# Optimization experiments

Hardware: AMD Instinct MI355X
Metric: run time of the kernel (lower is better)

Reference implementation:

```python
import jax, jax.numpy as jnp
import numpy as np


def _forward(x, conv_w, conv_b, lin_w, lin_b, W_in, conv1d_w, conv1d_b, W_x, W_dt, b_dt, A_log, Dp, W_out, We, be, Wa, ba, Wq, bq):
    B, _, H, Wd = x.shape
    E = conv_w.shape[0]
    # conv stem: Conv2d(k=3, pad=1) -> flatten(2) -> Linear(H*W -> img_size)
    z = jax.lax.conv_general_dilated(x, conv_w, (1, 1), [(1, 1), (1, 1)],
                                     dimension_numbers=('NCHW', 'OIHW', 'NCHW'))
    z = z + conv_b[None, :, None, None]
    z = z.reshape(B, E, H * Wd)                              # [B,E,HW]
    z = jnp.einsum('ben,mn->bem', z, lin_w) + lin_b          # [B,E,L]
    u = z.transpose(2, 0, 1)                                 # [L,B,E]: Mamba sees batch=L, seq=B
    # ---- Mamba block (mamba_ssm reference math) ----
    di = W_in.shape[0] // 2
    xz = u @ W_in.T                                          # [L,seq,2*di]
    xm, zg = xz[..., :di], xz[..., di:]
    K = conv1d_w.shape[-1]
    xc = jax.lax.conv_general_dilated(xm.transpose(0, 2, 1), conv1d_w, (1,), [(K - 1, 0)],
                                      dimension_numbers=('NCH', 'OIH', 'NCH'),
                                      feature_group_count=di)  # causal depthwise conv
    xs = jax.nn.silu((xc + conv1d_b[None, :, None]).transpose(0, 2, 1))  # [L,seq,di]
    dbl = xs @ W_x.T                                         # [L,seq,dt_rank+2S]
    dt_rank = W_dt.shape[1]
    S = A_log.shape[1]
    delta = jax.nn.softplus(dbl[..., :dt_rank] @ W_dt.T + b_dt)          # [L,seq,di]
    Bm = dbl[..., dt_rank:dt_rank + S]                       # [L,seq,S]
    Cm = dbl[..., dt_rank + S:]                              # [L,seq,S]
    A = -jnp.exp(A_log)                                      # [di,S]

    def step(h, t):
        d_t, b_t, c_t, x_t = t                               # [L,di],[L,S],[L,S],[L,di]
        h = jnp.exp(d_t[:, :, None] * A) * h + (d_t * x_t)[:, :, None] * b_t[:, None, :]
        return h, jnp.einsum('lds,ls->ld', h, c_t)

    h0 = jnp.zeros((u.shape[0], di, S), xs.dtype)
    _, ys = jax.lax.scan(step, h0, (delta.transpose(1, 0, 2), Bm.transpose(1, 0, 2),
                                    Cm.transpose(1, 0, 2), xs.transpose(1, 0, 2)))
    y = (ys.transpose(1, 0, 2) + xs * Dp) * jax.nn.silu(zg)  # [L,seq,di]
    out = y @ W_out.T                                        # [L,seq,E]
    feat = out[-1]                                           # [B,E] (last 'mamba batch' row)
    return feat @ We.T + be, feat @ Wa.T + ba, feat @ Wq.T + bq


def setup_inputs() -> dict:
    key = jax.random.key(0)
    ks = jax.random.split(key, 16)
    B, C, IMG, E, S, K = 512, 1, 32, 128, 256, 4
    di, dt_rank = 2 * E, 8
    sc = 0.02
    return {
        'x': jax.random.normal(ks[0], (B, C, IMG, IMG), jnp.float32),
        'conv_w': sc * jax.random.normal(ks[1], (E, C, 3, 3), jnp.float32),
        'conv_b': jnp.zeros((E,), jnp.float32),
        'lin_w': sc * jax.random.normal(ks[2], (IMG, IMG * IMG), jnp.float32),
        'lin_b': jnp.zeros((IMG,), jnp.float32),
        'W_in': sc * jax.random.normal(ks[3], (2 * di, E), jnp.float32),
        'conv1d_w': sc * jax.random.normal(ks[4], (di, 1, K), jnp.float32),
        'conv1d_b': jnp.zeros((di,), jnp.float32),
        'W_x': sc * jax.random.normal(ks[5], (dt_rank + 2 * S, di), jnp.float32),
        'W_dt': sc * jax.random.normal(ks[6], (di, dt_rank), jnp.float32),
        'b_dt': 0.1 * jax.random.normal(ks[7], (di,), jnp.float32),
        'A_log': jnp.log(jnp.broadcast_to(jnp.arange(1, S + 1, dtype=jnp.float32), (di, S))),
        'Dp': jnp.ones((di,), jnp.float32),
        'W_out': sc * jax.random.normal(ks[8], (E, di), jnp.float32),
        'We': sc * jax.random.normal(ks[9], (1, E), jnp.float32),
        'be': jnp.zeros((1,), jnp.float32),
        'Wa': sc * jax.random.normal(ks[10], (3, E), jnp.float32),
        'ba': jnp.zeros((3,), jnp.float32),
        'Wq': sc * jax.random.normal(ks[11], (4, E), jnp.float32),
        'bq': jnp.zeros((4,), jnp.float32),
    }


def reference(x, conv_w, conv_b, lin_w, lin_b, W_in, conv1d_w, conv1d_b, W_x, W_dt, b_dt, A_log, Dp, W_out, We, be, Wa, ba, Wq, bq):
    return _forward(x, conv_w, conv_b, lin_w, lin_b, W_in, conv1d_w, conv1d_b, W_x,
                    W_dt, b_dt, A_log, Dp, W_out, We, be, Wa, ba, Wq, bq)
```

## Files before the change

kernel.cpp:

```cpp
#include <hip/hip_runtime.h>
#include <math.h>

#define BATCH 512
#define E     128
#define DI    256
#define S     256
#define DTR   8
#define KCONV 4

__device__ __forceinline__ float silu_f(float v) {
    return v / (1.0f + __expf(-v));
}

__global__ __launch_bounds__(256) void k1_conv_lin(
    const float* __restrict__ x, const float* __restrict__ conv_w,
    const float* __restrict__ conv_b, const float* __restrict__ lin_w,
    const float* __restrict__ lin_b, float* __restrict__ u31)
{
    const int b = blockIdx.x;
    const int tid = threadIdx.x;
    __shared__ float lw[1024];
    __shared__ float red[10][4];
    __shared__ float Tsh[10];

    for (int i = tid; i < 1024; i += 256) lw[i] = lin_w[31 * 1024 + i];
    __syncthreads();

    float acc[10];
#pragma unroll
    for (int k = 0; k < 10; k++) acc[k] = 0.0f;

    const float* xb = x + (size_t)b * 1024;
    for (int p = tid; p < 1024; p += 256) {
        const float xv = xb[p];
        const int h = p >> 5, w = p & 31;
#pragma unroll
        for (int i = 0; i < 3; i++) {
            const int hh = h - (i - 1);
            if (hh < 0 || hh > 31) continue;
#pragma unroll
            for (int j = 0; j < 3; j++) {
                const int ww = w - (j - 1);
                if (ww < 0 || ww > 31) continue;
                acc[i * 3 + j] += xv * lw[hh * 32 + ww];
            }
        }
        acc[9] += lw[p];
    }

    const int wv = tid >> 6, ln = tid & 63;
#pragma unroll
    for (int k = 0; k < 10; k++) {
#pragma unroll
        for (int m = 1; m < 64; m <<= 1) acc[k] += __shfl_xor(acc[k], m, 64);
    }
    if (ln == 0) {
#pragma unroll
        for (int k = 0; k < 10; k++) red[k][wv] = acc[k];
    }
    __syncthreads();
    if (tid < 10) Tsh[tid] = red[tid][0] + red[tid][1] + red[tid][2] + red[tid][3];
    __syncthreads();

    if (tid < E) {
        const int e = tid;
        float v = lin_b[31] + conv_b[e] * Tsh[9];
#pragma unroll
        for (int k = 0; k < 9; k++) v += conv_w[e * 9 + k] * Tsh[k];
        u31[b * E + e] = v;
    }
}

__global__ __launch_bounds__(256) void k2a_win(
    const float* __restrict__ u31, const float* __restrict__ W_in,
    float* __restrict__ xm, float* __restrict__ zg)
{
    const int bb = blockIdx.x * 4;
    const int tid = threadIdx.x;
    __shared__ float u[4][E];
    for (int i = tid; i < 4 * E; i += 256) u[i >> 7][i & 127] = u31[bb * E + i];
    __syncthreads();

    const int jj = blockIdx.y * 256 + tid;
    float acc[4];
#pragma unroll
    for (int r = 0; r < 4; r++) acc[r] = 0.0f;
    const float* wrow = W_in + jj * E;
#pragma unroll 4
    for (int e = 0; e < E; e++) {
        const float w = wrow[e];
#pragma unroll
        for (int r = 0; r < 4; r++) acc[r] += w * u[r][e];
    }
    if (jj < 256) {
#pragma unroll
        for (int r = 0; r < 4; r++) xm[(bb + r) * DI + jj] = acc[r];
    } else {
#pragma unroll
        for (int r = 0; r < 4; r++) zg[(bb + r) * DI + (jj - 256)] = acc[r];
    }
}

__global__ __launch_bounds__(256) void k2b_conv_wx(
    const float* __restrict__ xm, const float* __restrict__ conv1d_w,
    const float* __restrict__ conv1d_b, const float* __restrict__ W_x,
    const float* __restrict__ W_dt, const float* __restrict__ b_dt,
    float* __restrict__ xs_g, float* __restrict__ delta_g,
    float* __restrict__ Bm, float* __restrict__ Cm)
{
    const int bb = blockIdx.x * 8;
    const int by = blockIdx.y;
    const int tid = threadIdx.x;
    __shared__ float xs[8][DI];
    __shared__ float dtin[8][8];

    for (int idx = tid; idx < 8 * DI; idx += 256) {
        const int r = idx >> 8, c = idx & 255;
        const int b = bb + r;
        float a = 0.0f;
#pragma unroll
        for (int k = 0; k < KCONV; k++) {
            const int src = b - 3 + k;
            if (src >= 0) a += xm[src * DI + c] * conv1d_w[c * KCONV + k];
        }
        a += conv1d_b[c];
        const float s = silu_f(a);
        xs[r][c] = s;
        if (by == 0) xs_g[b * DI + c] = s;
    }
    __syncthreads();

    for (int jj = by * 260 + tid; jj < (by + 1) * 260; jj += 256) {
        float acc[8];
#pragma unroll
        for (int r = 0; r < 8; r++) acc[r] = 0.0f;
        const float* wrow = W_x + jj * DI;
#pragma unroll 4
        for (int c = 0; c < DI; c++) {
            const float w = wrow[c];
#pragma unroll
            for (int r = 0; r < 8; r++) acc[r] += w * xs[r][c];
        }
#pragma unroll
        for (int r = 0; r < 8; r++) {
            const int b = bb + r;
            if (jj < DTR)          dtin[r][jj] = acc[r];
            else if (jj < DTR + S) Bm[b * S + (jj - DTR)] = acc[r];
            else                   Cm[b * S + (jj - DTR - S)] = acc[r];
        }
    }
    __syncthreads();

    if (by == 0) {
        const int d = tid;
        const float bd = b_dt[d];
#pragma unroll
        for (int r = 0; r < 8; r++) {
            float a = bd;
#pragma unroll
            for (int q = 0; q < DTR; q++) a += dtin[r][q] * W_dt[d * DTR + q];
            const float sp = (a > 20.0f) ? a : log1pf(__expf(a));
            delta_g[(bb + r) * DI + d] = sp;
        }
    }
}

template <int NCv>
__global__ __launch_bounds__(256) void k3a_local(
    const float* __restrict__ A_log, const float* __restrict__ delta,
    const float* __restrict__ xs, const float* __restrict__ Bm,
    const float* __restrict__ Cm, float* __restrict__ y,
    float* __restrict__ hloc, float* __restrict__ Dchunk)
{
    constexpr int TCv = BATCH / NCv;
    const int tid = threadIdx.x;
    const int wv = tid >> 6, ln = tid & 63;
    const int d = blockIdx.x * 4 + wv;
    const int c = blockIdx.y;
    const int s0 = ln * 4;
    const int t0 = c * TCv;

    const float4 al = *(const float4*)(A_log + d * S + s0);
    float4 A;
    A.x = -__expf(al.x); A.y = -__expf(al.y);
    A.z = -__expf(al.z); A.w = -__expf(al.w);

    float4 h = make_float4(0.f, 0.f, 0.f, 0.f);
    float cd = 0.0f;
    float pr[8];

    for (int tb = 0; tb < TCv; tb += 8) {
#pragma unroll
        for (int i = 0; i < 8; i++) {
            const int tt = t0 + tb + i;
            const float dd = delta[tt * DI + d];
            cd += dd;
            const float u = dd * xs[tt * DI + d];
            const float4 B = *(const float4*)(Bm + tt * S + s0);
            const float4 C = *(const float4*)(Cm + tt * S + s0);
            h.x = __expf(dd * A.x) * h.x + u * B.x;
            h.y = __expf(dd * A.y) * h.y + u * B.y;
            h.z = __expf(dd * A.z) * h.z + u * B.z;
            h.w = __expf(dd * A.w) * h.w + u * B.w;
            pr[i] = h.x * C.x + h.y * C.y + h.z * C.z + h.w * C.w;
        }
#pragma unroll
        for (int i = 0; i < 8; i++) {
#pragma unroll
            for (int m = 1; m < 64; m <<= 1) pr[i] += __shfl_xor(pr[i], m, 64);
        }
        if (ln == 0) {
#pragma unroll
            for (int i = 0; i < 8; i++) y[(t0 + tb + i) * DI + d] = pr[i];
        }
    }

    *(float4*)(hloc + ((size_t)(c * DI + d)) * S + s0) = h;
    if (ln == 0) Dchunk[c * DI + d] = cd;
}

template <int NCv>
__global__ __launch_bounds__(256) void k3b_carry(
    const float* __restrict__ A_log, const float* __restrict__ hloc,
    const float* __restrict__ Dchunk, float* __restrict__ hin)
{
    const int d = blockIdx.x;
    const int s = threadIdx.x;
    const float A = -__expf(A_log[d * S + s]);

    float h = 0.0f;
    float hf = hloc[((size_t)(0 * DI + d)) * S + s];
    float Dc = Dchunk[0 * DI + d];
    for (int c = 1; c < NCv; c++) {
        float hf_n = 0.0f, Dc_n = 0.0f;
        if (c < NCv - 1) {
            hf_n = hloc[((size_t)(c * DI + d)) * S + s];
            Dc_n = Dchunk[c * DI + d];
        }
        h = hf + __expf(A * Dc) * h;
        hin[((size_t)(c * DI + d)) * S + s] = h;
        hf = hf_n; Dc = Dc_n;
    }
}

template <int NCv>
__global__ __launch_bounds__(256) void k3c_fix(
    const float* __restrict__ A_log, const float* __restrict__ delta,
    const float* __restrict__ Cm, const float* __restrict__ hin,
    float* __restrict__ y)
{
    constexpr int TCv = BATCH / NCv;
    const int tid = threadIdx.x;
    const int wv = tid >> 6, ln = tid & 63;
    const int d = blockIdx.x * 4 + wv;
    const int c = blockIdx.y + 1;
    const int s0 = ln * 4;
    const int t0 = c * TCv;

    const float4 al = *(const float4*)(A_log + d * S + s0);
    float4 A;
    A.x = -__expf(al.x); A.y = -__expf(al.y);
    A.z = -__expf(al.z); A.w = -__expf(al.w);

    const float4 hi = *(const float4*)(hin + ((size_t)(c * DI + d)) * S + s0);

    float cd = 0.0f;
    float pr[8];

    for (int tb = 0; tb < TCv; tb += 8) {
#pragma unroll
        for (int i = 0; i < 8; i++) {
            const int tt = t0 + tb + i;
            const float dd = delta[tt * DI + d];
            cd += dd;
            const float4 C = *(const float4*)(Cm + tt * S + s0);
            const float fx = hi.x * __expf(cd * A.x);
            const float fy = hi.y * __expf(cd * A.y);
            const float fz = hi.z * __expf(cd * A.z);
            const float fw = hi.w * __expf(cd * A.w);
            pr[i] = fx * C.x + fy * C.y + fz * C.z + fw * C.w;
        }
#pragma unroll
        for (int i = 0; i < 8; i++) {
#pragma unroll
            for (int m = 1; m < 64; m <<= 1) pr[i] += __shfl_xor(pr[i], m, 64);
        }
        if (ln == 0) {
#pragma unroll
            for (int i = 0; i < 8; i++) {
                const int tt = t0 + tb + i;
                y[tt * DI + d] += pr[i];
            }
        }
    }
}

__global__ __launch_bounds__(256) void k4_heads(
    const float* __restrict__ y, const float* __restrict__ xs,
    const float* __restrict__ Dp, const float* __restrict__ zg,
    const float* __restrict__ W_out,
    const float* __restrict__ We, const float* __restrict__ be,
    const float* __restrict__ Wa, const float* __restrict__ ba,
    const float* __restrict__ Wq, const float* __restrict__ bq,
    float* __restrict__ out)
{
    const int b = blockIdx.x;
    const int tid = threadIdx.x;
    __shared__ float yf[DI];
    __shared__ float feat[E];

    const float z = zg[b * DI + tid];
    yf[tid] = (y[b * DI + tid] + xs[b * DI + tid] * Dp[tid]) * silu_f(z);
    __syncthreads();

    if (tid < E) {
        float a = 0.0f;
#pragma unroll 4
        for (int dd = 0; dd < DI; dd++) a += yf[dd] * W_out[tid * DI + dd];
        feat[tid] = a;
    }
    __syncthreads();

    if (tid < 8) {
        const float* wrow;
        float bias;
        int dst;
        if (tid == 0)      { wrow = We;                  bias = be[0];       dst = b; }
        else if (tid < 4)  { wrow = Wa + (tid - 1) * E;  bias = ba[tid - 1]; dst = 512 + b * 3 + (tid - 1); }
        else               { wrow = Wq + (tid - 4) * E;  bias = bq[tid - 4]; dst = 2048 + b * 4 + (tid - 4); }
        float a = bias;
#pragma unroll 4
        for (int e = 0; e < E; e++) a += feat[e] * wrow[e];
        out[dst] = a;
    }
}

template <int NCv>
static void launch_scan(const float* A_log, const float* delta, const float* xs,
                        const float* Bm, const float* Cm, float* y,
                        float* hloc, float* hin, float* Dchunk, hipStream_t stream)
{
    k3a_local<NCv><<<dim3(64, NCv), 256, 0, stream>>>(A_log, delta, xs, Bm, Cm, y, hloc, Dchunk);
    k3b_carry<NCv><<<256, 256, 0, stream>>>(A_log, hloc, Dchunk, hin);
    k3c_fix<NCv><<<dim3(64, NCv - 1), 256, 0, stream>>>(A_log, delta, Cm, hin, y);
}

extern "C" void kernel_launch(void* const* d_in, const int* in_sizes, int n_in,
                              void* d_out, int out_size, void* d_ws, size_t ws_size,
                              hipStream_t stream)
{
    const float* x        = (const float*)d_in[0];
    const float* conv_w   = (const float*)d_in[1];
    const float* conv_b   = (const float*)d_in[2];
    const float* lin_w    = (const float*)d_in[3];
    const float* lin_b    = (const float*)d_in[4];
    const float* W_in     = (const float*)d_in[5];
    const float* conv1d_w = (const float*)d_in[6];
    const float* conv1d_b = (const float*)d_in[7];
    const float* W_x      = (const float*)d_in[8];
    const float* W_dt     = (const float*)d_in[9];
    const float* b_dt     = (const float*)d_in[10];
    const float* A_log    = (const float*)d_in[11];
    const float* Dp       = (const float*)d_in[12];
    const float* W_out    = (const float*)d_in[13];
    const float* We       = (const float*)d_in[14];
    const float* be       = (const float*)d_in[15];
    const float* Wa       = (const float*)d_in[16];
    const float* ba       = (const float*)d_in[17];
    const float* Wq       = (const float*)d_in[18];
    const float* bq       = (const float*)d_in[19];
    float* out = (float*)d_out;

    float* ws = (float*)d_ws;
    float* u31   = ws;
    float* xm    = u31 + 512 * 128;
    float* zg    = xm  + 512 * 256;
    float* xs    = zg  + 512 * 256;
    float* delta = xs  + 512 * 256;
    float* Bm    = delta + 512 * 256;
    float* Cm    = Bm  + 512 * 256;
    float* y     = Cm  + 512 * 256;
    float* tail  = y   + 512 * 256;

    const size_t base_floats = (size_t)(tail - ws);

    k1_conv_lin<<<512, 256, 0, stream>>>(x, conv_w, conv_b, lin_w, lin_b, u31);
    k2a_win<<<dim3(128, 2), 256, 0, stream>>>(u31, W_in, xm, zg);
    k2b_conv_wx<<<dim3(64, 2), 256, 0, stream>>>(xm, conv1d_w, conv1d_b, W_x, W_dt, b_dt,
                                                 xs, delta, Bm, Cm);

    const size_t avail = ws_size / 4 - base_floats;
    if (avail >= (size_t)2 * 32 * DI * S + 32 * DI) {
        float* hloc = tail;
        float* hin  = hloc + (size_t)32 * DI * S;
        float* Dch  = hin  + (size_t)32 * DI * S;
        launch_scan<32>(A_log, delta, xs, Bm, Cm, y, hloc, hin, Dch, stream);
    } else if (avail >= (size_t)2 * 16 * DI * S + 16 * DI) {
        float* hloc = tail;
        float* hin  = hloc + (size_t)16 * DI * S;
        float* Dch  = hin  + (size_t)16 * DI * S;
        launch_scan<16>(A_log, delta, xs, Bm, Cm, y, hloc, hin, Dch, stream);
    } else {
        float* hloc = tail;
        float* hin  = hloc + (size_t)8 * DI * S;
        float* Dch  = hin  + (size_t)8 * DI * S;
        launch_scan<8>(A_log, delta, xs, Bm, Cm, y, hloc, hin, Dch, stream);
    }

    k4_heads<<<512, 256, 0, stream>>>(y, xs, Dp, zg, W_out, We, be, Wa, ba, Wq, bq, out);
}
```

Baseline: 200.3 us.

## Transpose weights on device for coalesced GEMV reads and re-grid projection kernels

Adds a per-call kernel that transposes W_in, W_x, W_dt, W_out and the conv1d weights into workspace, so the matvec loops read weight rows coalesced across threads instead of strided per-thread rows. It also re-grids k2a and k2b (more blocks, one output per thread with a row index per wave), processes two batch rows per block in the heads kernel, and vectorizes the conv stem loads with float4. The aim is better memory coalescing and occupancy in the small projection kernels. The cost is an extra launch plus transpose traffic on every call, and the reduced per-thread reuse of the shared-memory rows.

```diff
diff --git a/kernel.cpp b/kernel.cpp
--- a/kernel.cpp
+++ b/kernel.cpp
@@ -7,9 +7,31 @@
 #define S     256
 #define DTR   8
 #define KCONV 4
+#define JWX   520
 
 __device__ __forceinline__ float silu_f(float v) {
     return v / (1.0f + __expf(-v));
+}
+
+__global__ __launch_bounds__(256) void kT_transpose(
+    const float* __restrict__ W_in, const float* __restrict__ W_x,
+    const float* __restrict__ W_dt, const float* __restrict__ W_out,
+    const float* __restrict__ c1w,
+    float* __restrict__ W_inT, float* __restrict__ W_xT,
+    float* __restrict__ W_dtT, float* __restrict__ W_outT,
+    float* __restrict__ c1wT)
+{
+    const int bid = blockIdx.x;
+    const float* src; float* dst; int J, K, j0;
+    if (bid < 9)       { src = W_x;   dst = W_xT;   J = JWX; K = DI;  j0 = bid * 64; }
+    else if (bid < 17) { src = W_in;  dst = W_inT;  J = 512; K = E;   j0 = (bid - 9) * 64; }
+    else if (bid < 19) { src = W_out; dst = W_outT; J = E;   K = DI;  j0 = (bid - 17) * 64; }
+    else if (bid < 23) { src = W_dt;  dst = W_dtT;  J = DI;  K = DTR; j0 = (bid - 19) * 64; }
+    else               { src = c1w;   dst = c1wT;   J = DI;  K = KCONV; j0 = (bid - 23) * 64; }
+    const int j = j0 + (threadIdx.x & 63);
+    if (j >= J) return;
+    for (int c = threadIdx.x >> 6; c < K; c += 4)
+        dst[c * J + j] = src[j * K + c];
 }
 
 __global__ __launch_bounds__(256) void k1_conv_lin(
@@ -23,17 +45,22 @@
     __shared__ float red[10][4];
     __shared__ float Tsh[10];
 
-    for (int i = tid; i < 1024; i += 256) lw[i] = lin_w[31 * 1024 + i];
+    const float4 lv = ((const float4*)(lin_w + 31 * 1024))[tid];
+    ((float4*)lw)[tid] = lv;
     __syncthreads();
 
     float acc[10];
 #pragma unroll
     for (int k = 0; k < 10; k++) acc[k] = 0.0f;
 
-    const float* xb = x + (size_t)b * 1024;
-    for (int p = tid; p < 1024; p += 256) {
-        const float xv = xb[p];
-        const int h = p >> 5, w = p & 31;
+    const float4 xv = ((const float4*)(x + (size_t)b * 1024))[tid];
+    const int p0 = tid * 4;
+    const int h = p0 >> 5, w0 = p0 & 31;
+    const float xa[4] = {xv.x, xv.y, xv.z, xv.w};
+#pragma unroll
+    for (int k = 0; k < 4; k++) {
+        const float xval = xa[k];
+        const int w = w0 + k;
 #pragma unroll
         for (int i = 0; i < 3; i++) {
             const int hh = h - (i - 1);
@@ -42,11 +69,11 @@
             for (int j = 0; j < 3; j++) {
                 const int ww = w - (j - 1);
                 if (ww < 0 || ww > 31) continue;
-                acc[i * 3 + j] += xv * lw[hh * 32 + ww];
+                acc[i * 3 + j] += xval * lw[hh * 32 + ww];
             }
         }
-        acc[9] += lw[p];
-    }
+    }
+    acc[9] = lv.x + lv.y + lv.z + lv.w;
 
     const int wv = tid >> 6, ln = tid & 63;
 #pragma unroll
@@ -72,7 +99,7 @@
 }
 
 __global__ __launch_bounds__(256) void k2a_win(
-    const float* __restrict__ u31, const float* __restrict__ W_in,
+    const float* __restrict__ u31, const float* __restrict__ W_inT,
     float* __restrict__ xm, float* __restrict__ zg)
 {
     const int bb = blockIdx.x * 4;
@@ -81,86 +108,67 @@
     for (int i = tid; i < 4 * E; i += 256) u[i >> 7][i & 127] = u31[bb * E + i];
     __syncthreads();
 
-    const int jj = blockIdx.y * 256 + tid;
-    float acc[4];
-#pragma unroll
-    for (int r = 0; r < 4; r++) acc[r] = 0.0f;
-    const float* wrow = W_in + jj * E;
-#pragma unroll 4
-    for (int e = 0; e < E; e++) {
-        const float w = wrow[e];
-#pragma unroll
-        for (int r = 0; r < 4; r++) acc[r] += w * u[r][e];
-    }
-    if (jj < 256) {
-#pragma unroll
-        for (int r = 0; r < 4; r++) xm[(bb + r) * DI + jj] = acc[r];
-    } else {
-#pragma unroll
-        for (int r = 0; r < 4; r++) zg[(bb + r) * DI + (jj - 256)] = acc[r];
-    }
+    const int r = tid >> 6;
+    const int j = blockIdx.y * 64 + (tid & 63);
+    float a = 0.0f;
+#pragma unroll 8
+    for (int e = 0; e < E; e++) a += u[r][e] * W_inT[e * 512 + j];
+    if (j < 256) xm[(bb + r) * DI + j] = a;
+    else         zg[(bb + r) * DI + (j - 256)] = a;
 }
 
 __global__ __launch_bounds__(256) void k2b_conv_wx(
-    const float* __restrict__ xm, const float* __restrict__ conv1d_w,
-    const float* __restrict__ conv1d_b, const float* __restrict__ W_x,
-    const float* __restrict__ W_dt, const float* __restrict__ b_dt,
+    const float* __restrict__ xm, const float* __restrict__ c1wT,
+    const float* __restrict__ conv1d_b, const float* __restrict__ W_xT,
+    const float* __restrict__ W_dtT, const float* __restrict__ b_dt,
     float* __restrict__ xs_g, float* __restrict__ delta_g,
     float* __restrict__ Bm, float* __restrict__ Cm)
 {
-    const int bb = blockIdx.x * 8;
-    const int by = blockIdx.y;
-    const int tid = threadIdx.x;
-    __shared__ float xs[8][DI];
-    __shared__ float dtin[8][8];
-
-    for (int idx = tid; idx < 8 * DI; idx += 256) {
+    const int bb = blockIdx.x * 4;
+    const int g = blockIdx.y;
+    const int tid = threadIdx.x;
+    __shared__ float xs[4][DI];
+    __shared__ float dtin[4][8];
+
+    for (int idx = tid; idx < 4 * DI; idx += 256) {
         const int r = idx >> 8, c = idx & 255;
         const int b = bb + r;
         float a = 0.0f;
 #pragma unroll
         for (int k = 0; k < KCONV; k++) {
             const int src = b - 3 + k;
-            if (src >= 0) a += xm[src * DI + c] * conv1d_w[c * KCONV + k];
+            if (src >= 0) a += xm[src * DI + c] * c1wT[k * DI + c];
         }
         a += conv1d_b[c];
         const float s = silu_f(a);
         xs[r][c] = s;
-        if (by == 0) xs_g[b * DI + c] = s;
-    }
-    __syncthreads();
-
-    for (int jj = by * 260 + tid; jj < (by + 1) * 260; jj += 256) {
-        float acc[8];
-#pragma unroll
-        for (int r = 0; r < 8; r++) acc[r] = 0.0f;
-        const float* wrow = W_x + jj * DI;
-#pragma unroll 4
-        for (int c = 0; c < DI; c++) {
-            const float w = wrow[c];
-#pragma unroll
-            for (int r = 0; r < 8; r++) acc[r] += w * xs[r][c];
-        }
-#pragma unroll
-        for (int r = 0; r < 8; r++) {
-            const int b = bb + r;
-            if (jj < DTR)          dtin[r][jj] = acc[r];
-            else if (jj < DTR + S) Bm[b * S + (jj - DTR)] = acc[r];
-            else                   Cm[b * S + (jj - DTR - S)] = acc[r];
-        }
-    }
-    __syncthreads();
-
-    if (by == 0) {
+        if (g == 0) xs_g[b * DI + c] = s;
+    }
+    __syncthreads();
+
+    const int r = tid >> 6;
+    const int j = g * 64 + (tid & 63);
+    if (j < JWX) {
+        float a = 0.0f;
+#pragma unroll 8
+        for (int c = 0; c < DI; c++) a += xs[r][c] * W_xT[c * JWX + j];
+        const int b = bb + r;
+        if (j < DTR)          dtin[r][j] = a;
+        else if (j < DTR + S) Bm[b * S + (j - DTR)] = a;
+        else                  Cm[b * S + (j - DTR - S)] = a;
+    }
+    __syncthreads();
+
+    if (g == 0) {
         const int d = tid;
         const float bd = b_dt[d];
 #pragma unroll
-        for (int r = 0; r < 8; r++) {
+        for (int r2 = 0; r2 < 4; r2++) {
             float a = bd;
 #pragma unroll
-            for (int q = 0; q < DTR; q++) a += dtin[r][q] * W_dt[d * DTR + q];
+            for (int q = 0; q < DTR; q++) a += dtin[r2][q] * W_dtT[q * DI + d];
             const float sp = (a > 20.0f) ? a : log1pf(__expf(a));
-            delta_g[(bb + r) * DI + d] = sp;
+            delta_g[(bb + r2) * DI + d] = sp;
         }
     }
 }
@@ -298,39 +306,46 @@
 __global__ __launch_bounds__(256) void k4_heads(
     const float* __restrict__ y, const float* __restrict__ xs,
     const float* __restrict__ Dp, const float* __restrict__ zg,
-    const float* __restrict__ W_out,
+    const float* __restrict__ W_outT,
     const float* __restrict__ We, const float* __restrict__ be,
     const float* __restrict__ Wa, const float* __restrict__ ba,
     const float* __restrict__ Wq, const float* __restrict__ bq,
     float* __restrict__ out)
 {
-    const int b = blockIdx.x;
-    const int tid = threadIdx.x;
-    __shared__ float yf[DI];
-    __shared__ float feat[E];
-
-    const float z = zg[b * DI + tid];
-    yf[tid] = (y[b * DI + tid] + xs[b * DI + tid] * Dp[tid]) * silu_f(z);
-    __syncthreads();
-
-    if (tid < E) {
+    const int bb = blockIdx.x * 2;
+    const int tid = threadIdx.x;
+    __shared__ float yf[2][DI];
+    __shared__ float feat[2][E];
+
+    for (int idx = tid; idx < 2 * DI; idx += 256) {
+        const int r = idx >> 8, c = idx & 255;
+        const int b = bb + r;
+        const float z = zg[b * DI + c];
+        yf[r][c] = (y[b * DI + c] + xs[b * DI + c] * Dp[c]) * silu_f(z);
+    }
+    __syncthreads();
+
+    {
+        const int r = tid >> 7, e = tid & 127;
         float a = 0.0f;
-#pragma unroll 4
-        for (int dd = 0; dd < DI; dd++) a += yf[dd] * W_out[tid * DI + dd];
-        feat[tid] = a;
-    }
-    __syncthreads();
-
-    if (tid < 8) {
+#pragma unroll 8
+        for (int dd = 0; dd < DI; dd++) a += yf[r][dd] * W_outT[dd * E + e];
+        feat[r][e] = a;
+    }
+    __syncthreads();
+
+    if (tid < 16) {
+        const int r = tid >> 3, hd = tid & 7;
+        const int b = bb + r;
         const float* wrow;
         float bias;
         int dst;
-        if (tid == 0)      { wrow = We;                  bias = be[0];       dst = b; }
-        else if (tid < 4)  { wrow = Wa + (tid - 1) * E;  bias = ba[tid - 1]; dst = 512 + b * 3 + (tid - 1); }
-        else               { wrow = Wq + (tid - 4) * E;  bias = bq[tid - 4]; dst = 2048 + b * 4 + (tid - 4); }
+        if (hd == 0)      { wrow = We;                 bias = be[0];      dst = b; }
+        else if (hd < 4)  { wrow = Wa + (hd - 1) * E;  bias = ba[hd - 1]; dst = 512 + b * 3 + (hd - 1); }
+        else              { wrow = Wq + (hd - 4) * E;  bias = bq[hd - 4]; dst = 2048 + b * 4 + (hd - 4); }
         float a = bias;
 #pragma unroll 4
-        for (int e = 0; e < E; e++) a += feat[e] * wrow[e];
+        for (int e = 0; e < E; e++) a += feat[r][e] * wrow[e];
         out[dst] = a;
     }
 }
@@ -380,14 +395,21 @@
     float* Bm    = delta + 512 * 256;
     float* Cm    = Bm  + 512 * 256;
     float* y     = Cm  + 512 * 256;
-    float* tail  = y   + 512 * 256;
+    float* W_inT = y   + 512 * 256;
+    float* W_xT  = W_inT + 128 * 512;
+    float* W_dtT = W_xT  + 256 * JWX;
+    float* W_outT= W_dtT + 8 * 256;
+    float* c1wT  = W_outT+ 256 * 128;
+    float* tail  = c1wT  + 4 * 256;
 
     const size_t base_floats = (size_t)(tail - ws);
 
+    kT_transpose<<<27, 256, 0, stream>>>(W_in, W_x, W_dt, W_out, conv1d_w,
+                                         W_inT, W_xT, W_dtT, W_outT, c1wT);
     k1_conv_lin<<<512, 256, 0, stream>>>(x, conv_w, conv_b, lin_w, lin_b, u31);
-    k2a_win<<<dim3(128, 2), 256, 0, stream>>>(u31, W_in, xm, zg);
-    k2b_conv_wx<<<dim3(64, 2), 256, 0, stream>>>(xm, conv1d_w, conv1d_b, W_x, W_dt, b_dt,
-                                                 xs, delta, Bm, Cm);
+    k2a_win<<<dim3(128, 8), 256, 0, stream>>>(u31, W_inT, xm, zg);
+    k2b_conv_wx<<<dim3(128, 9), 256, 0, stream>>>(xm, c1wT, conv1d_b, W_xT, W_dtT, b_dt,
+                                                  xs, delta, Bm, Cm);
 
     const size_t avail = ws_size / 4 - base_floats;
     if (avail >= (size_t)2 * 32 * DI * S + 32 * DI) {
@@ -407,5 +429,5 @@
         launch_scan<8>(A_log, delta, xs, Bm, Cm, y, hloc, hin, Dch, stream);
     }
 
-    k4_heads<<<512, 256, 0, stream>>>(y, xs, Dp, zg, W_out, We, be, Wa, ba, Wq, bq, out);
-}
+    k4_heads<<<256, 256, 0, stream>>>(y, xs, Dp, zg, W_outT, We, be, Wa, ba, Wq, bq, out);
+}
```

Result: faster. 185.3 us (-7.5%).
